# Kernel tuning notes

Measured on AMD Instinct MI355X. Metric: run time of the kernel, lower is better.

## Reference

```python
import jax, jax.numpy as jnp
import numpy as np

B, C, H, W = 16, 512, 64, 64
HEADS = 8
DIL = 2  # dilation of the 3x3 depthwise conv (padding == dilation -> shape preserving)


def setup_inputs() -> dict:
    key = jax.random.key(0)
    ks = jax.random.split(key, 4)
    x = jax.random.normal(ks[0], (B, C, H, W), jnp.float32)
    # kaiming-normal-ish scales (fan_out, relu)
    w_qkv = jax.random.normal(ks[1], (3 * C, C), jnp.float32) * (2.0 / C) ** 0.5  # 1x1 conv weight
    w_dw = jax.random.normal(ks[2], (C, 3, 3), jnp.float32) * (2.0 / 9.0) ** 0.5  # depthwise 3x3
    w_out = jax.random.normal(ks[3], (C, C), jnp.float32) * (2.0 / C) ** 0.5      # 1x1 conv weight
    temperature = jnp.sqrt(jnp.asarray(C // HEADS, jnp.float32))                  # init sqrt(dim_per_head)
    return {"x": x, "w_qkv": w_qkv, "w_dw": w_dw, "w_out": w_out, "temperature": temperature}


def _dw_conv(y, w_dw):
    # depthwise dilated 3x3 conv, padding=dilation -> same spatial size
    rhs = w_dw[:, None, :, :]  # [C,1,3,3]
    return jax.lax.conv_general_dilated(
        y, rhs, window_strides=(1, 1), padding=((DIL, DIL), (DIL, DIL)),
        rhs_dilation=(DIL, DIL), feature_group_count=y.shape[1],
        dimension_numbers=("NCHW", "OIHW", "NCHW"))


def reference(x, w_qkv, w_dw, w_out, temperature):
    b, c, h, w = x.shape
    n = h * w
    d = c // HEADS
    # 1x1 qkv projection (bias-free conv == einsum)
    qkv = jnp.einsum("oc,bchw->bohw", w_qkv, x)  # [B,3C,H,W]
    q, k, v = jnp.split(qkv, 3, axis=1)
    # same depthwise conv applied to q,k,v: fold into batch, conv once
    qkv3 = _dw_conv(jnp.concatenate([q, k, v], axis=0), w_dw)  # [3B,C,H,W]
    q, k, v = jnp.split(qkv3, 3, axis=0)
    q = q.reshape(b, HEADS, d, n)
    k = k.reshape(b, HEADS, d, n)
    v = v.reshape(b, HEADS, d, n)
    # L2 normalize along the per-head channel dim (dim=2), eps=1e-12 like F.normalize
    l2 = lambda t: t / jnp.maximum(jnp.linalg.norm(t, axis=2, keepdims=True), 1e-12)
    q = l2(q)
    k = l2(k)
    # cross-covariance attention: [B,heads,d,d]
    attn = jnp.einsum("bhdn,bhen->bhde", q, k) / jnp.maximum(temperature, 1e-5)
    attn = jax.nn.softmax(attn, axis=-1)
    # dropout is identity in eval mode
    out = jnp.einsum("bhde,bhen->bhdn", attn, v).reshape(b, c, h, w)
    return jnp.einsum("oc,bchw->bohw", w_out, out)
```

## Files before the change

kernel.cpp:

```cpp
#include <hip/hip_runtime.h>

typedef __attribute__((ext_vector_type(8))) short bf16x8;
typedef __attribute__((ext_vector_type(8))) unsigned short ushort8;
typedef __attribute__((ext_vector_type(4))) float f32x4;
typedef __attribute__((ext_vector_type(2))) float f32x2;
typedef __attribute__((ext_vector_type(4))) unsigned int u32x4;
typedef __attribute__((ext_vector_type(2))) unsigned int u32x2;

__device__ __forceinline__ float bf2f(unsigned short u) {
  union { unsigned int i; float f; } v; v.i = ((unsigned int)u) << 16; return v.f;
}
__device__ __forceinline__ float asf(unsigned int u) {
  union { unsigned int i; float f; } v; v.i = u; return v.f;
}
__device__ __forceinline__ unsigned short f2bf(float f) {
  union { float f; unsigned int i; } v; v.f = f;
  unsigned int u = v.i;
  return (unsigned short)((u + 0x7FFFu + ((u >> 16) & 1u)) >> 16);
}
__device__ __forceinline__ void gload16(const void* g, void* l) {
  __builtin_amdgcn_global_load_lds(
      (const __attribute__((address_space(1))) void*)g,
      (__attribute__((address_space(3))) void*)l, 16, 0, 0);
}

__global__ __launch_bounds__(256) void cvt_f32_bf16(const float* __restrict__ s,
                                                    unsigned short* __restrict__ d, int n) {
  int i = blockIdx.x * 256 + threadIdx.x;
  if (i < n) d[i] = f2bf(s[i]);
}

__global__ __launch_bounds__(256) void transpose_x(const float* __restrict__ x,
                                                   unsigned short* __restrict__ xt) {
  __shared__ float tile[64][65];
  const int b = blockIdx.z, ct = blockIdx.y, nt = blockIdx.x;
  const int t = threadIdx.x;
  const int r0 = t >> 6, col = t & 63;
  const float* src = x + ((size_t)b * 512 + ct * 64) * 4096 + nt * 64;
#pragma unroll
  for (int i = 0; i < 16; ++i) {
    int r = i * 4 + r0;
    tile[r][col] = src[(size_t)r * 4096 + col];
  }
  __syncthreads();
  unsigned short* dst = xt + ((size_t)b * 4096 + nt * 64) * 512 + ct * 64;
  const int c2 = (t & 31) * 2;
  const int nsub = t >> 5;
#pragma unroll
  for (int i = 0; i < 8; ++i) {
    int n = i * 8 + nsub;
    unsigned int p;
    asm("v_cvt_pk_bf16_f32 %0, %1, %2" : "=v"(p) : "v"(tile[c2][n]), "v"(tile[c2 + 1][n]));
    *(unsigned int*)(dst + (size_t)n * 512 + c2) = p;
  }
}

__global__ __launch_bounds__(512, 1) void gemm_qkv_8ph(const unsigned short* __restrict__ A,
                                                       const unsigned short* __restrict__ B,
                                                       unsigned short* __restrict__ C) {
  __shared__ unsigned short lA[2][256 * 64];
  __shared__ unsigned short lB[2][256 * 64];
  const int gx = gridDim.x;
  const int nwg = gx * gridDim.y;
  int flat = blockIdx.x + gx * blockIdx.y;
  flat = (flat & 7) * (nwg >> 3) + (flat >> 3);
  const int bx = flat % gx;
  const int by = flat / gx;
  const size_t m0 = (size_t)by * 256;
  const size_t n0 = (size_t)bx * 256;

  const int t = threadIdx.x;
  const int lane = t & 63;
  const int wid = t >> 6;
  const int wm = wid >> 2, wn = wid & 3;
  const int ro = lane & 15, kq = lane >> 4;

  const int srow = t >> 3;
  const int sslot = t & 7;
  const int kslot = sslot ^ (srow & 7);

  auto stageA = [&](int kt, int h, int bbuf) {
    char* d = (char*)(&lA[bbuf][0]) + ((h * 128 + srow) * 64 + sslot * 8) * 2;
    const unsigned short* g = A + (m0 + h * 128 + srow) * 512 + kt * 64 + kslot * 8;
    gload16(g, d);
    gload16(g + (size_t)64 * 512, d + 64 * 128);
  };
  auto stageB = [&](int kt, int h, int bbuf) {
    char* d = (char*)(&lB[bbuf][0]) + ((h * 128 + srow) * 64 + sslot * 8) * 2;
    const unsigned short* g = B + (n0 + h * 128 + srow) * 512 + kt * 64 + kslot * 8;
    gload16(g, d);
    gload16(g + (size_t)64 * 512, d + 64 * 128);
  };

  f32x4 acc[8][4] = {};

  stageA(0, 0, 0); stageA(0, 1, 0);
  stageB(0, 0, 0); stageB(0, 1, 0);
  stageA(1, 0, 1); stageA(1, 1, 1);
  asm volatile("s_waitcnt vmcnt(4)" ::: "memory");
  __builtin_amdgcn_s_barrier();

#pragma unroll 1
  for (int kt = 0; kt < 8; ++kt) {
    const int c = kt & 1;
    const unsigned short* pa = &lA[c][0];
    const unsigned short* pb = &lB[c][0];
    const int slot0 = kq ^ (ro & 7);
    const int slot1 = (4 + kq) ^ (ro & 7);

    bf16x8 a0[8], a1[8], b0, b1, b2, b3;
#pragma unroll
    for (int i = 0; i < 8; ++i)
      a0[i] = *(const bf16x8*)&pa[(wm * 128 + i * 16 + ro) * 64 + slot0 * 8];
    b0 = *(const bf16x8*)&pb[(wn * 64 + 0 * 16 + ro) * 64 + slot0 * 8];
    b1 = *(const bf16x8*)&pb[(wn * 64 + 1 * 16 + ro) * 64 + slot0 * 8];
    if (kt + 1 < 8) stageB(kt + 1, 0, c ^ 1);
    asm volatile("" ::: "memory");
    __builtin_amdgcn_s_barrier();
    asm volatile("s_waitcnt lgkmcnt(0)" ::: "memory");
    __builtin_amdgcn_s_setprio(1);
#pragma unroll
    for (int i = 0; i < 8; ++i) {
      acc[i][0] = __builtin_amdgcn_mfma_f32_16x16x32_bf16(a0[i], b0, acc[i][0], 0, 0, 0);
      acc[i][1] = __builtin_amdgcn_mfma_f32_16x16x32_bf16(a0[i], b1, acc[i][1], 0, 0, 0);
    }
    __builtin_amdgcn_s_setprio(0);

    b2 = *(const bf16x8*)&pb[(wn * 64 + 2 * 16 + ro) * 64 + slot0 * 8];
    b3 = *(const bf16x8*)&pb[(wn * 64 + 3 * 16 + ro) * 64 + slot0 * 8];
    if (kt + 1 < 8) stageB(kt + 1, 1, c ^ 1);
    asm volatile("" ::: "memory");
    __builtin_amdgcn_s_barrier();
    asm volatile("s_waitcnt lgkmcnt(0)" ::: "memory");
    __builtin_amdgcn_s_setprio(1);
#pragma unroll
    for (int i = 0; i < 8; ++i) {
      acc[i][2] = __builtin_amdgcn_mfma_f32_16x16x32_bf16(a0[i], b2, acc[i][2], 0, 0, 0);
      acc[i][3] = __builtin_amdgcn_mfma_f32_16x16x32_bf16(a0[i], b3, acc[i][3], 0, 0, 0);
    }
    __builtin_amdgcn_s_setprio(0);

#pragma unroll
    for (int i = 0; i < 8; ++i)
      a1[i] = *(const bf16x8*)&pa[(wm * 128 + i * 16 + ro) * 64 + slot1 * 8];
    b0 = *(const bf16x8*)&pb[(wn * 64 + 0 * 16 + ro) * 64 + slot1 * 8];
    b1 = *(const bf16x8*)&pb[(wn * 64 + 1 * 16 + ro) * 64 + slot1 * 8];
    asm volatile("s_waitcnt lgkmcnt(0)" ::: "memory");
    __builtin_amdgcn_s_barrier();
    __builtin_amdgcn_s_setprio(1);
#pragma unroll
    for (int i = 0; i < 8; ++i) {
      acc[i][0] = __builtin_amdgcn_mfma_f32_16x16x32_bf16(a1[i], b0, acc[i][0], 0, 0, 0);
      acc[i][1] = __builtin_amdgcn_mfma_f32_16x16x32_bf16(a1[i], b1, acc[i][1], 0, 0, 0);
    }
    __builtin_amdgcn_s_setprio(0);

    b2 = *(const bf16x8*)&pb[(wn * 64 + 2 * 16 + ro) * 64 + slot1 * 8];
    b3 = *(const bf16x8*)&pb[(wn * 64 + 3 * 16 + ro) * 64 + slot1 * 8];
    if (kt + 2 < 8) { stageA(kt + 2, 0, c); stageA(kt + 2, 1, c); }
    asm volatile("s_waitcnt lgkmcnt(0)" ::: "memory");
    if (kt < 6)       asm volatile("s_waitcnt vmcnt(4)" ::: "memory");
    else if (kt == 6) asm volatile("s_waitcnt vmcnt(0)" ::: "memory");
    __builtin_amdgcn_s_barrier();
    __builtin_amdgcn_s_setprio(1);
#pragma unroll
    for (int i = 0; i < 8; ++i) {
      acc[i][2] = __builtin_amdgcn_mfma_f32_16x16x32_bf16(a1[i], b2, acc[i][2], 0, 0, 0);
      acc[i][3] = __builtin_amdgcn_mfma_f32_16x16x32_bf16(a1[i], b3, acc[i][3], 0, 0, 0);
    }
    __builtin_amdgcn_s_setprio(0);
  }

#pragma unroll
  for (int i = 0; i < 8; ++i)
#pragma unroll
    for (int j = 0; j < 4; ++j)
#pragma unroll
      for (int r = 0; r < 4; ++r) {
        size_t row = m0 + wm * 128 + i * 16 + (kq << 2) + r;
        size_t col = n0 + wn * 64 + j * 16 + ro;
        C[row * 1536 + col] = f2bf(acc[i][j][r]);
      }
}

template <bool BF16OUT>
__global__ __launch_bounds__(256) void gemm_bt(const unsigned short* __restrict__ A,
                                               const unsigned short* __restrict__ B,
                                               void* __restrict__ Cv, int K, int ldc,
                                               size_t sA, size_t sB, size_t sC) {
  __shared__ unsigned short lA[2][128 * 32];
  __shared__ unsigned short lB[2][128 * 32];
  const int gx = gridDim.x, gy = gridDim.y;
  const int nwg = gx * gy * gridDim.z;
  int flat = blockIdx.x + gx * (blockIdx.y + gy * blockIdx.z);
  flat = (flat & 7) * (nwg >> 3) + (flat >> 3);
  const int bx = flat % gx;
  const int rem = flat / gx;
  const int by = rem % gy;
  const int bz = rem / gy;

  const int t = threadIdx.x;
  const int lane = t & 63;
  const int wv = t >> 6, wr = wv >> 1, wc = wv & 1;
  const size_t m0 = (size_t)by * 128;
  const size_t n0 = (size_t)bx * 128;
  A += (size_t)bz * sA;
  B += (size_t)bz * sB;
  const unsigned short* ga = A + (m0 + (t >> 2)) * (size_t)K + (t & 3) * 8;
  const unsigned short* gb = B + (n0 + (t >> 2)) * (size_t)K + (t & 3) * 8;
  const size_t gstep = (size_t)64 * K;

  f32x4 acc[4][4] = {};

  auto stage = [&](int kt, int bbuf) {
    const unsigned short* pa = ga + kt * 32;
    const unsigned short* pb = gb + kt * 32;
    char* da = (char*)(&lA[bbuf][0]) + t * 16;
    char* db = (char*)(&lB[bbuf][0]) + t * 16;
    gload16(pa, da);
    gload16(pa + gstep, da + 4096);
    gload16(pb, db);
    gload16(pb + gstep, db + 4096);
  };

  const int nk = K >> 5;
  stage(0, 0);
  __syncthreads();
  int buf = 0;
  for (int kt = 0; kt < nk; ++kt) {
    if (kt + 1 < nk) stage(kt + 1, buf ^ 1);
    const unsigned short* pa = &lA[buf][0];
    const unsigned short* pb = &lB[buf][0];
    const int ro = lane & 15, ko = (lane >> 4) * 8;
    bf16x8 af[4], bv[4];
#pragma unroll
    for (int i = 0; i < 4; ++i) af[i] = *(const bf16x8*)&pa[(wr * 64 + i * 16 + ro) * 32 + ko];
#pragma unroll
    for (int i = 0; i < 4; ++i) bv[i] = *(const bf16x8*)&pb[(wc * 64 + i * 16 + ro) * 32 + ko];
#pragma unroll
    for (int i = 0; i < 4; ++i)
#pragma unroll
      for (int j = 0; j < 4; ++j)
        acc[i][j] = __builtin_amdgcn_mfma_f32_16x16x32_bf16(af[i], bv[j], acc[i][j], 0, 0, 0);
    __syncthreads();
    buf ^= 1;
  }

  if constexpr (BF16OUT) {
    unsigned short* C = (unsigned short*)Cv + (size_t)bz * sC;
#pragma unroll
    for (int i = 0; i < 4; ++i)
#pragma unroll
      for (int j = 0; j < 4; ++j)
#pragma unroll
        for (int r = 0; r < 4; ++r) {
          size_t row = m0 + wr * 64 + i * 16 + ((lane >> 4) << 2) + r;
          size_t col = n0 + wc * 64 + j * 16 + (lane & 15);
          C[row * (size_t)ldc + col] = f2bf(acc[i][j][r]);
        }
  } else {
    float* C = (float*)Cv + (size_t)bz * sC;
#pragma unroll
    for (int i = 0; i < 4; ++i)
#pragma unroll
      for (int j = 0; j < 4; ++j)
#pragma unroll
        for (int r = 0; r < 4; ++r) {
          size_t row = m0 + wr * 64 + i * 16 + ((lane >> 4) << 2) + r;
          size_t col = n0 + wc * 64 + j * 16 + (lane & 15);
          C[row * (size_t)ldc + col] = acc[i][j][r];
        }
  }
}

struct Row3h { u32x2 v[3]; };

__global__ __launch_bounds__(256) void dwconv_norm(const unsigned short* __restrict__ Y,
                                                   const float* __restrict__ wdw,
                                                   unsigned short* __restrict__ Qb,
                                                   unsigned short* __restrict__ Kb,
                                                   unsigned short* __restrict__ Vb) {
  const int t = threadIdx.x, lane = t & 63, wv = t >> 6;
  const int bid = blockIdx.x;
  const int lbid = (bid & 7) * 384 + (bid >> 3);
  const int wid = lbid * 4 + wv;
  const int sub = wid & 3;
  const int x = (wid >> 2) & 63;
  const int grp = wid >> 8;
  const int par = sub >> 1, chhalf = sub & 1;
  const int b = grp / 3, part = grp - b * 3;
  const int c0 = chhalf * 256 + (lane >> 4) * 64 + (lane & 15) * 4;

  f32x2 wa[9], wb[9];
  {
    float qw[36];
    const float* wp = wdw + c0 * 9;
#pragma unroll
    for (int i = 0; i < 9; ++i) {
      f32x4 q = *(const f32x4*)(wp + i * 4);
      qw[i * 4 + 0] = q[0]; qw[i * 4 + 1] = q[1];
      qw[i * 4 + 2] = q[2]; qw[i * 4 + 3] = q[3];
    }
#pragma unroll
    for (int tap = 0; tap < 9; ++tap) {
      wa[tap] = (f32x2){qw[tap], qw[9 + tap]};
      wb[tap] = (f32x2){qw[18 + tap], qw[27 + tap]};
    }
  }

  const size_t ybase = (size_t)b * 4096 * 1536 + part * 512 + c0;
  const bool okm = (x >= 2), okp = (x <= 61);
  const int xm = okm ? x - 2 : x;
  const int xp = okp ? x + 2 : x;

  auto loadrow = [&](int yy) -> Row3h {
    Row3h r;
    const bool oky = ((unsigned)yy < 64u);
    const int yyc = oky ? yy : 0;
    const size_t rb = ybase + (size_t)(yyc * 64) * 1536;
    u32x2 a = *(const u32x2*)(Y + rb + (size_t)xm * 1536);
    u32x2 c = *(const u32x2*)(Y + rb + (size_t)x * 1536);
    u32x2 d = *(const u32x2*)(Y + rb + (size_t)xp * 1536);
    r.v[0] = a & ((oky && okm) ? 0xFFFFFFFFu : 0u);
    r.v[1] = c & (oky ? 0xFFFFFFFFu : 0u);
    r.v[2] = d & ((oky && okp) ? 0xFFFFFFFFu : 0u);
    return r;
  };

  Row3h W[4];
#pragma unroll
  for (int xt = 0; xt < 3; ++xt) W[0].v[xt] = (u32x2)(0u);
  W[1] = loadrow(par);
  W[2] = loadrow(par + 2);
  W[3] = loadrow(par + 4);

  unsigned short* dst0 = (part == 0 ? Qb : (part == 1 ? Kb : Vb)) +
                         ((size_t)b * 4096 + x) * 512 + c0;

#pragma unroll
  for (int i = 0; i < 32; ++i) {
    const int y = par + 2 * i;
    f32x2 a01 = (f32x2){0.f, 0.f}, a23 = (f32x2){0.f, 0.f};
#pragma unroll
    for (int r = 0; r < 3; ++r) {
      const Row3h& R = W[(i + r) & 3];
#pragma unroll
      for (int xt = 0; xt < 3; ++xt) {
        const int tap = r * 3 + xt;
        const u32x2 v = R.v[xt];
        f32x2 lo = (f32x2){asf(v[0] << 16), asf(v[0] & 0xFFFF0000u)};
        f32x2 hi = (f32x2){asf(v[1] << 16), asf(v[1] & 0xFFFF0000u)};
        a01 += lo * wa[tap];
        a23 += hi * wb[tap];
      }
    }
    if (part < 2) {
      f32x2 s2 = a01 * a01 + a23 * a23;
      float ss = s2[0] + s2[1];
      ss += __shfl_xor(ss, 1);
      ss += __shfl_xor(ss, 2);
      ss += __shfl_xor(ss, 4);
      ss += __shfl_xor(ss, 8);
      const float rcp = 1.f / fmaxf(sqrtf(ss), 1e-12f);
      a01 *= rcp; a23 *= rcp;
    }
    unsigned int p0, p1;
    asm("v_cvt_pk_bf16_f32 %0, %1, %2" : "=v"(p0) : "v"(a01[0]), "v"(a01[1]));
    asm("v_cvt_pk_bf16_f32 %0, %1, %2" : "=v"(p1) : "v"(a23[0]), "v"(a23[1]));
    u32x2 pk; pk[0] = p0; pk[1] = p1;
    *(u32x2*)(dst0 + (size_t)y * 64 * 512) = pk;
    if (i < 30) W[i & 3] = loadrow(y + 6);
  }
}

__global__ __launch_bounds__(256) void attn_partial(const unsigned short* __restrict__ Qb,
                                                    const unsigned short* __restrict__ Kb,
                                                    float* __restrict__ Spart) {
  __shared__ unsigned short sQ[4][64][72];
  __shared__ unsigned short sK[4][64][72];
  const int t = threadIdx.x, lane = t & 63, wv = t >> 6;
  const int bh = blockIdx.x >> 2;
  const int s = (blockIdx.x & 3) * 4 + wv;
  const int b = bh >> 3, h = bh & 7;
  const unsigned short* qbase = Qb + ((size_t)b * 4096) * 512 + h * 64;
  const unsigned short* kbase = Kb + ((size_t)b * 4096) * 512 + h * 64;
  f32x4 acc[4][4] = {};
  for (int ch = 0; ch < 4; ++ch) {
    const int n0 = s * 256 + ch * 64;
    const unsigned short* qp = qbase + (size_t)(n0 + lane) * 512;
    const unsigned short* kp = kbase + (size_t)(n0 + lane) * 512;
    ushort8 qv[8], kv[8];
#pragma unroll
    for (int v = 0; v < 8; ++v) qv[v] = *(const ushort8*)(qp + v * 8);
#pragma unroll
    for (int v = 0; v < 8; ++v) kv[v] = *(const ushort8*)(kp + v * 8);
#pragma unroll
    for (int v = 0; v < 8; ++v)
#pragma unroll
      for (int j = 0; j < 8; ++j) {
        sQ[wv][v * 8 + j][lane] = qv[v][j];
        sK[wv][v * 8 + j][lane] = kv[v][j];
      }
    __syncthreads();
    const int ro = lane & 15, ko = (lane >> 4) * 8;
#pragma unroll
    for (int ks = 0; ks < 2; ++ks) {
      bf16x8 af[4], bv[4];
#pragma unroll
      for (int i = 0; i < 4; ++i) af[i] = *(const bf16x8*)&sQ[wv][i * 16 + ro][ks * 32 + ko];
#pragma unroll
      for (int i = 0; i < 4; ++i) bv[i] = *(const bf16x8*)&sK[wv][i * 16 + ro][ks * 32 + ko];
#pragma unroll
      for (int i = 0; i < 4; ++i)
#pragma unroll
        for (int j = 0; j < 4; ++j)
          acc[i][j] = __builtin_amdgcn_mfma_f32_16x16x32_bf16(af[i], bv[j], acc[i][j], 0, 0, 0);
    }
    __syncthreads();
  }
  float* dst = Spart + ((size_t)bh * 16 + s) * 4096;
#pragma unroll
  for (int i = 0; i < 4; ++i)
#pragma unroll
    for (int j = 0; j < 4; ++j)
#pragma unroll
      for (int r = 0; r < 4; ++r) {
        int d = i * 16 + ((lane >> 4) << 2) + r;
        int e = j * 16 + (lane & 15);
        dst[d * 64 + e] = acc[i][j][r];
      }
}

__global__ __launch_bounds__(256) void softmax_attn(const float* __restrict__ Spart,
                                                    const float* __restrict__ tptr,
                                                    unsigned short* __restrict__ attn) {
  const int bh = blockIdx.x, t = threadIdx.x;
  const int d = t >> 2, eb = (t & 3) << 4;
  const float inv_t = 1.f / fmaxf(tptr[0], 1e-5f);
  float v[16];
#pragma unroll
  for (int i = 0; i < 16; ++i) v[i] = 0.f;
  for (int s = 0; s < 16; ++s) {
    const f32x4* p = (const f32x4*)(Spart + ((size_t)bh * 16 + s) * 4096 + d * 64 + eb);
#pragma unroll
    for (int i = 0; i < 4; ++i) {
      f32x4 q = p[i];
      v[i * 4 + 0] += q[0]; v[i * 4 + 1] += q[1];
      v[i * 4 + 2] += q[2]; v[i * 4 + 3] += q[3];
    }
  }
  float mx = -1e30f;
#pragma unroll
  for (int i = 0; i < 16; ++i) { v[i] *= inv_t; mx = fmaxf(mx, v[i]); }
  mx = fmaxf(mx, __shfl_xor(mx, 1));
  mx = fmaxf(mx, __shfl_xor(mx, 2));
  float sm = 0.f;
#pragma unroll
  for (int i = 0; i < 16; ++i) { v[i] = __expf(v[i] - mx); sm += v[i]; }
  sm += __shfl_xor(sm, 1);
  sm += __shfl_xor(sm, 2);
  const float r = 1.f / sm;
  ushort8 pk0, pk1;
#pragma unroll
  for (int i = 0; i < 8; ++i) { pk0[i] = f2bf(v[i] * r); pk1[i] = f2bf(v[8 + i] * r); }
  ushort8* dst = (ushort8*)(attn + (size_t)bh * 4096 + d * 64 + eb);
  dst[0] = pk0; dst[1] = pk1;
}

__global__ __launch_bounds__(256) void make_w2(const unsigned short* __restrict__ attn,
                                               const float* __restrict__ w_out,
                                               unsigned short* __restrict__ w2) {
  __shared__ float sA[4096];
  const int bx = blockIdx.x;
  const int bh = bx >> 1, half = bx & 1;
  const int b = bh >> 3, h = bh & 7;
  const int t = threadIdx.x;
  for (int i = t; i < 4096; i += 256) sA[i] = bf2f(attn[(size_t)bh * 4096 + i]);
  __syncthreads();
  const int o = half * 256 + t;
  float w[64];
  const float* wp = w_out + (size_t)o * 512 + h * 64;
#pragma unroll
  for (int i = 0; i < 64; i += 4) {
    f32x4 q = *(const f32x4*)(wp + i);
    w[i] = q[0]; w[i + 1] = q[1]; w[i + 2] = q[2]; w[i + 3] = q[3];
  }
  unsigned short* dst = w2 + ((size_t)b * 512 + o) * 512 + h * 64;
#pragma unroll 1
  for (int eg = 0; eg < 8; ++eg) {
    ushort8 pk;
#pragma unroll
    for (int ee = 0; ee < 8; ++ee) {
      const int e = eg * 8 + ee;
      float acc = 0.f;
#pragma unroll
      for (int dd = 0; dd < 64; ++dd) acc += w[dd] * sA[dd * 64 + e];
      pk[ee] = f2bf(acc);
    }
    *(ushort8*)(dst + eg * 8) = pk;
  }
}

extern "C" void kernel_launch(void* const* d_in, const int* in_sizes, int n_in,
                              void* d_out, int out_size, void* d_ws, size_t ws_size,
                              hipStream_t stream) {
  const float* x     = (const float*)d_in[0];
  const float* w_qkv = (const float*)d_in[1];
  const float* w_dw  = (const float*)d_in[2];
  const float* w_out = (const float*)d_in[3];
  const float* temp  = (const float*)d_in[4];
  float* out = (float*)d_out;

  char* ws = (char*)d_ws;
  const size_t MB = 1024 * 1024;
  unsigned short* Xt    = (unsigned short*)(ws);
  float*          Spart = (float*)(ws);
  unsigned short* attn  = (unsigned short*)(ws + 32 * MB);
  unsigned short* w2    = (unsigned short*)(ws + 33 * MB);
  unsigned short* Y     = (unsigned short*)(ws + 64 * MB);
  unsigned short* Qb    = (unsigned short*)(ws + 256 * MB);
  unsigned short* Kb    = (unsigned short*)(ws + 320 * MB);
  unsigned short* Vb    = (unsigned short*)(ws + 384 * MB);
  unsigned short* Wq    = (unsigned short*)(ws + 448 * MB);

  cvt_f32_bf16<<<3072, 256, 0, stream>>>(w_qkv, Wq, 1536 * 512);
  transpose_x<<<dim3(64, 8, 16), 256, 0, stream>>>(x, Xt);
  gemm_qkv_8ph<<<dim3(6, 256), 512, 0, stream>>>(Xt, Wq, Y);
  dwconv_norm<<<3072, 256, 0, stream>>>(Y, w_dw, Qb, Kb, Vb);
  attn_partial<<<512, 256, 0, stream>>>(Qb, Kb, Spart);
  softmax_attn<<<128, 256, 0, stream>>>(Spart, temp, attn);
  make_w2<<<256, 256, 0, stream>>>(attn, w_out, w2);
  gemm_bt<false><<<dim3(32, 4, 16), 256, 0, stream>>>(
      w2, Vb, out, 512, 4096,
      (size_t)512 * 512, (size_t)4096 * 512, (size_t)512 * 4096);
}
```

Baseline: 413.0 us.

## Compute two dilated-conv columns per wave to share horizontal tap loads

Each wave in the depthwise dilated conv now produces two output columns (x0 and x0+2) over half the rows, loading four input columns per row instead of three per column. Horizontal input reuse cuts global loads per output from 3 to 2 per row, and the split into row halves keeps the total wave count the same. In exchange each lane holds more live registers (two accumulator sets, 12 loaded vectors) and needs extra halo row loads at each row-half boundary.

```diff
diff --git a/kernel.cpp b/kernel.cpp
--- a/kernel.cpp
+++ b/kernel.cpp
@@ -273,7 +273,7 @@
   }
 }
 
-struct Row3h { u32x2 v[3]; };
+struct Row4 { u32x2 v[4]; };
 
 __global__ __launch_bounds__(256) void dwconv_norm(const unsigned short* __restrict__ Y,
                                                    const float* __restrict__ wdw,
@@ -284,11 +284,12 @@
   const int bid = blockIdx.x;
   const int lbid = (bid & 7) * 384 + (bid >> 3);
   const int wid = lbid * 4 + wv;
-  const int sub = wid & 3;
-  const int x = (wid >> 2) & 63;
+  const int sub = wid & 255;
   const int grp = wid >> 8;
-  const int par = sub >> 1, chhalf = sub & 1;
+  const int pair = sub >> 3;
+  const int par = (sub >> 2) & 1, chhalf = (sub >> 1) & 1, rowhalf = sub & 1;
   const int b = grp / 3, part = grp - b * 3;
+  const int x0 = (pair >> 1) * 4 + (pair & 1);
   const int c0 = chhalf * 256 + (lane >> 4) * 64 + (lane & 15) * 4;
 
   f32x2 wa[9], wb[9];
@@ -309,67 +310,86 @@
   }
 
   const size_t ybase = (size_t)b * 4096 * 1536 + part * 512 + c0;
-  const bool okm = (x >= 2), okp = (x <= 61);
-  const int xm = okm ? x - 2 : x;
-  const int xp = okp ? x + 2 : x;
-
-  auto loadrow = [&](int yy) -> Row3h {
-    Row3h r;
+  const bool okm = (x0 >= 2), okp = (x0 + 4 <= 63);
+  const int cm = okm ? x0 - 2 : x0;
+  const int cp = okp ? x0 + 4 : x0;
+
+  auto loadrow = [&](int yy) -> Row4 {
+    Row4 r;
     const bool oky = ((unsigned)yy < 64u);
     const int yyc = oky ? yy : 0;
     const size_t rb = ybase + (size_t)(yyc * 64) * 1536;
-    u32x2 a = *(const u32x2*)(Y + rb + (size_t)xm * 1536);
-    u32x2 c = *(const u32x2*)(Y + rb + (size_t)x * 1536);
-    u32x2 d = *(const u32x2*)(Y + rb + (size_t)xp * 1536);
+    u32x2 a = *(const u32x2*)(Y + rb + (size_t)cm * 1536);
+    u32x2 c = *(const u32x2*)(Y + rb + (size_t)x0 * 1536);
+    u32x2 d = *(const u32x2*)(Y + rb + (size_t)(x0 + 2) * 1536);
+    u32x2 e = *(const u32x2*)(Y + rb + (size_t)cp * 1536);
     r.v[0] = a & ((oky && okm) ? 0xFFFFFFFFu : 0u);
     r.v[1] = c & (oky ? 0xFFFFFFFFu : 0u);
-    r.v[2] = d & ((oky && okp) ? 0xFFFFFFFFu : 0u);
+    r.v[2] = d & (oky ? 0xFFFFFFFFu : 0u);
+    r.v[3] = e & ((oky && okp) ? 0xFFFFFFFFu : 0u);
     return r;
   };
 
-  Row3h W[4];
-#pragma unroll
-  for (int xt = 0; xt < 3; ++xt) W[0].v[xt] = (u32x2)(0u);
-  W[1] = loadrow(par);
-  W[2] = loadrow(par + 2);
-  W[3] = loadrow(par + 4);
-
-  unsigned short* dst0 = (part == 0 ? Qb : (part == 1 ? Kb : Vb)) +
-                         ((size_t)b * 4096 + x) * 512 + c0;
-
-#pragma unroll
-  for (int i = 0; i < 32; ++i) {
-    const int y = par + 2 * i;
-    f32x2 a01 = (f32x2){0.f, 0.f}, a23 = (f32x2){0.f, 0.f};
+  const int y0 = par + rowhalf * 32;
+  Row4 W[3];
+  W[0] = loadrow(y0 - 2);
+  W[1] = loadrow(y0);
+  W[2] = loadrow(y0 + 2);
+
+  unsigned short* dstA = (part == 0 ? Qb : (part == 1 ? Kb : Vb)) +
+                         ((size_t)b * 4096 + x0) * 512 + c0;
+  unsigned short* dstB = dstA + (size_t)2 * 512;
+
+#pragma unroll
+  for (int i = 0; i < 16; ++i) {
+    const int y = y0 + 2 * i;
+    f32x2 A01 = (f32x2){0.f, 0.f}, A23 = (f32x2){0.f, 0.f};
+    f32x2 B01 = (f32x2){0.f, 0.f}, B23 = (f32x2){0.f, 0.f};
 #pragma unroll
     for (int r = 0; r < 3; ++r) {
-      const Row3h& R = W[(i + r) & 3];
-#pragma unroll
-      for (int xt = 0; xt < 3; ++xt) {
-        const int tap = r * 3 + xt;
+      const Row4& R = W[(i + r) % 3];
+#pragma unroll
+      for (int xt = 0; xt < 4; ++xt) {
         const u32x2 v = R.v[xt];
         f32x2 lo = (f32x2){asf(v[0] << 16), asf(v[0] & 0xFFFF0000u)};
         f32x2 hi = (f32x2){asf(v[1] << 16), asf(v[1] & 0xFFFF0000u)};
-        a01 += lo * wa[tap];
-        a23 += hi * wb[tap];
+        if (xt < 3) {
+          const int tap = r * 3 + xt;
+          A01 += lo * wa[tap];
+          A23 += hi * wb[tap];
+        }
+        if (xt >= 1) {
+          const int tap = r * 3 + xt - 1;
+          B01 += lo * wa[tap];
+          B23 += hi * wb[tap];
+        }
       }
     }
     if (part < 2) {
-      f32x2 s2 = a01 * a01 + a23 * a23;
-      float ss = s2[0] + s2[1];
-      ss += __shfl_xor(ss, 1);
-      ss += __shfl_xor(ss, 2);
-      ss += __shfl_xor(ss, 4);
-      ss += __shfl_xor(ss, 8);
-      const float rcp = 1.f / fmaxf(sqrtf(ss), 1e-12f);
-      a01 *= rcp; a23 *= rcp;
-    }
-    unsigned int p0, p1;
-    asm("v_cvt_pk_bf16_f32 %0, %1, %2" : "=v"(p0) : "v"(a01[0]), "v"(a01[1]));
-    asm("v_cvt_pk_bf16_f32 %0, %1, %2" : "=v"(p1) : "v"(a23[0]), "v"(a23[1]));
-    u32x2 pk; pk[0] = p0; pk[1] = p1;
-    *(u32x2*)(dst0 + (size_t)y * 64 * 512) = pk;
-    if (i < 30) W[i & 3] = loadrow(y + 6);
+      f32x2 sa = A01 * A01 + A23 * A23;
+      f32x2 sb = B01 * B01 + B23 * B23;
+      float ssa = sa[0] + sa[1];
+      float ssb = sb[0] + sb[1];
+#pragma unroll
+      for (int m = 1; m <= 8; m <<= 1) {
+        ssa += __shfl_xor(ssa, m);
+        ssb += __shfl_xor(ssb, m);
+      }
+      const float ra = 1.f / fmaxf(sqrtf(ssa), 1e-12f);
+      const float rb2 = 1.f / fmaxf(sqrtf(ssb), 1e-12f);
+      A01 *= ra; A23 *= ra;
+      B01 *= rb2; B23 *= rb2;
+    }
+    unsigned int p0, p1, q0, q1;
+    asm("v_cvt_pk_bf16_f32 %0, %1, %2" : "=v"(p0) : "v"(A01[0]), "v"(A01[1]));
+    asm("v_cvt_pk_bf16_f32 %0, %1, %2" : "=v"(p1) : "v"(A23[0]), "v"(A23[1]));
+    asm("v_cvt_pk_bf16_f32 %0, %1, %2" : "=v"(q0) : "v"(B01[0]), "v"(B01[1]));
+    asm("v_cvt_pk_bf16_f32 %0, %1, %2" : "=v"(q1) : "v"(B23[0]), "v"(B23[1]));
+    u32x2 pkA; pkA[0] = p0; pkA[1] = p1;
+    u32x2 pkB; pkB[0] = q0; pkB[1] = q1;
+    *(u32x2*)(dstA + (size_t)y * 64 * 512) = pkA;
+    *(u32x2*)(dstB + (size_t)y * 64 * 512) = pkB;
+    if (i < 15) W[i % 3] = loadrow(y + 4);
   }
 }
 
```

After: 403.3 us. -2.3%, faster.

## Reuse 256x256 8-phase GEMM for output projection and widen dwconv per-thread tiles

Applied to the files above, without the earlier changes.

The final batched output GEMM now runs on the 256x256 eight-phase pipelined MFMA kernel used for the QKV projection, replacing the simpler 128x128 double-buffered kernel, which was generalised with batch strides and an fp32 output path. The depthwise conv kernel now has each wave compute four output columns (stride two) over half the rows, loading six input columns per row so neighbouring taps are shared and redundant global loads drop. The grid is halved to match. The trade-offs are more registers per thread in the conv and fewer workgroups for the output GEMM (512), which may lower occupancy and load balance.

```diff
diff --git a/kernel.cpp b/kernel.cpp
--- a/kernel.cpp
+++ b/kernel.cpp
@@ -55,19 +55,25 @@
   }
 }
 
-__global__ __launch_bounds__(512, 1) void gemm_qkv_8ph(const unsigned short* __restrict__ A,
-                                                       const unsigned short* __restrict__ B,
-                                                       unsigned short* __restrict__ C) {
+template <bool BF16OUT>
+__global__ __launch_bounds__(512, 1) void gemm256_8ph(const unsigned short* __restrict__ A,
+                                                      const unsigned short* __restrict__ B,
+                                                      void* __restrict__ Cv, int ldc,
+                                                      size_t sA, size_t sB, size_t sC) {
   __shared__ unsigned short lA[2][256 * 64];
   __shared__ unsigned short lB[2][256 * 64];
-  const int gx = gridDim.x;
-  const int nwg = gx * gridDim.y;
-  int flat = blockIdx.x + gx * blockIdx.y;
+  const int gx = gridDim.x, gy = gridDim.y;
+  const int nwg = gx * gy * gridDim.z;
+  int flat = blockIdx.x + gx * (blockIdx.y + gy * blockIdx.z);
   flat = (flat & 7) * (nwg >> 3) + (flat >> 3);
   const int bx = flat % gx;
-  const int by = flat / gx;
+  const int rem = flat / gx;
+  const int by = rem % gy;
+  const int bz = rem / gy;
   const size_t m0 = (size_t)by * 256;
   const size_t n0 = (size_t)bx * 256;
+  A += (size_t)bz * sA;
+  B += (size_t)bz * sB;
 
   const int t = threadIdx.x;
   const int lane = t & 63;
@@ -171,109 +177,34 @@
     __builtin_amdgcn_s_setprio(0);
   }
 
-#pragma unroll
-  for (int i = 0; i < 8; ++i)
-#pragma unroll
-    for (int j = 0; j < 4; ++j)
-#pragma unroll
-      for (int r = 0; r < 4; ++r) {
-        size_t row = m0 + wm * 128 + i * 16 + (kq << 2) + r;
-        size_t col = n0 + wn * 64 + j * 16 + ro;
-        C[row * 1536 + col] = f2bf(acc[i][j][r]);
-      }
-}
-
-template <bool BF16OUT>
-__global__ __launch_bounds__(256) void gemm_bt(const unsigned short* __restrict__ A,
-                                               const unsigned short* __restrict__ B,
-                                               void* __restrict__ Cv, int K, int ldc,
-                                               size_t sA, size_t sB, size_t sC) {
-  __shared__ unsigned short lA[2][128 * 32];
-  __shared__ unsigned short lB[2][128 * 32];
-  const int gx = gridDim.x, gy = gridDim.y;
-  const int nwg = gx * gy * gridDim.z;
-  int flat = blockIdx.x + gx * (blockIdx.y + gy * blockIdx.z);
-  flat = (flat & 7) * (nwg >> 3) + (flat >> 3);
-  const int bx = flat % gx;
-  const int rem = flat / gx;
-  const int by = rem % gy;
-  const int bz = rem / gy;
-
-  const int t = threadIdx.x;
-  const int lane = t & 63;
-  const int wv = t >> 6, wr = wv >> 1, wc = wv & 1;
-  const size_t m0 = (size_t)by * 128;
-  const size_t n0 = (size_t)bx * 128;
-  A += (size_t)bz * sA;
-  B += (size_t)bz * sB;
-  const unsigned short* ga = A + (m0 + (t >> 2)) * (size_t)K + (t & 3) * 8;
-  const unsigned short* gb = B + (n0 + (t >> 2)) * (size_t)K + (t & 3) * 8;
-  const size_t gstep = (size_t)64 * K;
-
-  f32x4 acc[4][4] = {};
-
-  auto stage = [&](int kt, int bbuf) {
-    const unsigned short* pa = ga + kt * 32;
-    const unsigned short* pb = gb + kt * 32;
-    char* da = (char*)(&lA[bbuf][0]) + t * 16;
-    char* db = (char*)(&lB[bbuf][0]) + t * 16;
-    gload16(pa, da);
-    gload16(pa + gstep, da + 4096);
-    gload16(pb, db);
-    gload16(pb + gstep, db + 4096);
-  };
-
-  const int nk = K >> 5;
-  stage(0, 0);
-  __syncthreads();
-  int buf = 0;
-  for (int kt = 0; kt < nk; ++kt) {
-    if (kt + 1 < nk) stage(kt + 1, buf ^ 1);
-    const unsigned short* pa = &lA[buf][0];
-    const unsigned short* pb = &lB[buf][0];
-    const int ro = lane & 15, ko = (lane >> 4) * 8;
-    bf16x8 af[4], bv[4];
-#pragma unroll
-    for (int i = 0; i < 4; ++i) af[i] = *(const bf16x8*)&pa[(wr * 64 + i * 16 + ro) * 32 + ko];
-#pragma unroll
-    for (int i = 0; i < 4; ++i) bv[i] = *(const bf16x8*)&pb[(wc * 64 + i * 16 + ro) * 32 + ko];
-#pragma unroll
-    for (int i = 0; i < 4; ++i)
+  if constexpr (BF16OUT) {
+    unsigned short* C = (unsigned short*)Cv + (size_t)0 * sC;
+#pragma unroll
+    for (int i = 0; i < 8; ++i)
 #pragma unroll
       for (int j = 0; j < 4; ++j)
-        acc[i][j] = __builtin_amdgcn_mfma_f32_16x16x32_bf16(af[i], bv[j], acc[i][j], 0, 0, 0);
-    __syncthreads();
-    buf ^= 1;
-  }
-
-  if constexpr (BF16OUT) {
-    unsigned short* C = (unsigned short*)Cv + (size_t)bz * sC;
-#pragma unroll
-    for (int i = 0; i < 4; ++i)
-#pragma unroll
-      for (int j = 0; j < 4; ++j)
 #pragma unroll
         for (int r = 0; r < 4; ++r) {
-          size_t row = m0 + wr * 64 + i * 16 + ((lane >> 4) << 2) + r;
-          size_t col = n0 + wc * 64 + j * 16 + (lane & 15);
+          size_t row = m0 + wm * 128 + i * 16 + (kq << 2) + r;
+          size_t col = n0 + wn * 64 + j * 16 + ro;
           C[row * (size_t)ldc + col] = f2bf(acc[i][j][r]);
         }
   } else {
     float* C = (float*)Cv + (size_t)bz * sC;
 #pragma unroll
-    for (int i = 0; i < 4; ++i)
+    for (int i = 0; i < 8; ++i)
 #pragma unroll
       for (int j = 0; j < 4; ++j)
 #pragma unroll
         for (int r = 0; r < 4; ++r) {
-          size_t row = m0 + wr * 64 + i * 16 + ((lane >> 4) << 2) + r;
-          size_t col = n0 + wc * 64 + j * 16 + (lane & 15);
+          size_t row = m0 + wm * 128 + i * 16 + (kq << 2) + r;
+          size_t col = n0 + wn * 64 + j * 16 + ro;
           C[row * (size_t)ldc + col] = acc[i][j][r];
         }
   }
 }
 
-struct Row3h { u32x2 v[3]; };
+struct Row6 { u32x2 v[6]; };
 
 __global__ __launch_bounds__(256) void dwconv_norm(const unsigned short* __restrict__ Y,
                                                    const float* __restrict__ wdw,
@@ -282,13 +213,14 @@
                                                    unsigned short* __restrict__ Vb) {
   const int t = threadIdx.x, lane = t & 63, wv = t >> 6;
   const int bid = blockIdx.x;
-  const int lbid = (bid & 7) * 384 + (bid >> 3);
+  const int lbid = (bid & 7) * 192 + (bid >> 3);
   const int wid = lbid * 4 + wv;
-  const int sub = wid & 3;
-  const int x = (wid >> 2) & 63;
-  const int grp = wid >> 8;
-  const int par = sub >> 1, chhalf = sub & 1;
+  const int sub = wid & 127;
+  const int grp = wid >> 7;
+  const int base = sub >> 3;
+  const int par = (sub >> 2) & 1, chhalf = (sub >> 1) & 1, rowhalf = sub & 1;
   const int b = grp / 3, part = grp - b * 3;
+  const int x0 = (base >> 1) * 8 + (base & 1);
   const int c0 = chhalf * 256 + (lane >> 4) * 64 + (lane & 15) * 4;
 
   f32x2 wa[9], wb[9];
@@ -309,67 +241,80 @@
   }
 
   const size_t ybase = (size_t)b * 4096 * 1536 + part * 512 + c0;
-  const bool okm = (x >= 2), okp = (x <= 61);
-  const int xm = okm ? x - 2 : x;
-  const int xp = okp ? x + 2 : x;
-
-  auto loadrow = [&](int yy) -> Row3h {
-    Row3h r;
+  const bool okm = (x0 >= 2), okp = (x0 + 8 <= 63);
+  int xc[6];
+  xc[0] = okm ? x0 - 2 : x0;
+#pragma unroll
+  for (int j = 1; j < 5; ++j) xc[j] = x0 - 2 + 2 * j;
+  xc[5] = okp ? x0 + 8 : x0;
+
+  auto loadrow = [&](int yy) -> Row6 {
+    Row6 r;
     const bool oky = ((unsigned)yy < 64u);
     const int yyc = oky ? yy : 0;
     const size_t rb = ybase + (size_t)(yyc * 64) * 1536;
-    u32x2 a = *(const u32x2*)(Y + rb + (size_t)xm * 1536);
-    u32x2 c = *(const u32x2*)(Y + rb + (size_t)x * 1536);
-    u32x2 d = *(const u32x2*)(Y + rb + (size_t)xp * 1536);
-    r.v[0] = a & ((oky && okm) ? 0xFFFFFFFFu : 0u);
-    r.v[1] = c & (oky ? 0xFFFFFFFFu : 0u);
-    r.v[2] = d & ((oky && okp) ? 0xFFFFFFFFu : 0u);
+#pragma unroll
+    for (int j = 0; j < 6; ++j) {
+      u32x2 v = *(const u32x2*)(Y + rb + (size_t)xc[j] * 1536);
+      bool ok = oky && !(j == 0 && !okm) && !(j == 5 && !okp);
+      r.v[j] = v & (ok ? 0xFFFFFFFFu : 0u);
+    }
     return r;
   };
 
-  Row3h W[4];
-#pragma unroll
-  for (int xt = 0; xt < 3; ++xt) W[0].v[xt] = (u32x2)(0u);
-  W[1] = loadrow(par);
-  W[2] = loadrow(par + 2);
-  W[3] = loadrow(par + 4);
+  const int y0 = par + rowhalf * 32;
+  Row6 W[3];
+  W[0] = loadrow(y0 - 2);
+  W[1] = loadrow(y0);
+  W[2] = loadrow(y0 + 2);
 
   unsigned short* dst0 = (part == 0 ? Qb : (part == 1 ? Kb : Vb)) +
-                         ((size_t)b * 4096 + x) * 512 + c0;
-
-#pragma unroll
-  for (int i = 0; i < 32; ++i) {
-    const int y = par + 2 * i;
-    f32x2 a01 = (f32x2){0.f, 0.f}, a23 = (f32x2){0.f, 0.f};
+                         ((size_t)b * 4096 + x0) * 512 + c0;
+
+#pragma unroll
+  for (int i = 0; i < 16; ++i) {
+    const int y = y0 + 2 * i;
+    f32x2 A01[4], A23[4];
+#pragma unroll
+    for (int o = 0; o < 4; ++o) { A01[o] = (f32x2){0.f, 0.f}; A23[o] = (f32x2){0.f, 0.f}; }
 #pragma unroll
     for (int r = 0; r < 3; ++r) {
-      const Row3h& R = W[(i + r) & 3];
-#pragma unroll
-      for (int xt = 0; xt < 3; ++xt) {
-        const int tap = r * 3 + xt;
-        const u32x2 v = R.v[xt];
+      const Row6& R = W[(i + r) % 3];
+#pragma unroll
+      for (int j = 0; j < 6; ++j) {
+        const u32x2 v = R.v[j];
         f32x2 lo = (f32x2){asf(v[0] << 16), asf(v[0] & 0xFFFF0000u)};
         f32x2 hi = (f32x2){asf(v[1] << 16), asf(v[1] & 0xFFFF0000u)};
-        a01 += lo * wa[tap];
-        a23 += hi * wb[tap];
+#pragma unroll
+        for (int o = 0; o < 4; ++o) {
+          const int xt = j - o;
+          if (xt >= 0 && xt < 3) {
+            const int tap = r * 3 + xt;
+            A01[o] += lo * wa[tap];
+            A23[o] += hi * wb[tap];
+          }
+        }
       }
     }
-    if (part < 2) {
-      f32x2 s2 = a01 * a01 + a23 * a23;
-      float ss = s2[0] + s2[1];
-      ss += __shfl_xor(ss, 1);
-      ss += __shfl_xor(ss, 2);
-      ss += __shfl_xor(ss, 4);
-      ss += __shfl_xor(ss, 8);
-      const float rcp = 1.f / fmaxf(sqrtf(ss), 1e-12f);
-      a01 *= rcp; a23 *= rcp;
-    }
-    unsigned int p0, p1;
-    asm("v_cvt_pk_bf16_f32 %0, %1, %2" : "=v"(p0) : "v"(a01[0]), "v"(a01[1]));
-    asm("v_cvt_pk_bf16_f32 %0, %1, %2" : "=v"(p1) : "v"(a23[0]), "v"(a23[1]));
-    u32x2 pk; pk[0] = p0; pk[1] = p1;
-    *(u32x2*)(dst0 + (size_t)y * 64 * 512) = pk;
-    if (i < 30) W[i & 3] = loadrow(y + 6);
+#pragma unroll
+    for (int o = 0; o < 4; ++o) {
+      if (part < 2) {
+        f32x2 s2 = A01[o] * A01[o] + A23[o] * A23[o];
+        float ss = s2[0] + s2[1];
+        ss += __shfl_xor(ss, 1);
+        ss += __shfl_xor(ss, 2);
+        ss += __shfl_xor(ss, 4);
+        ss += __shfl_xor(ss, 8);
+        const float rcp = 1.f / fmaxf(sqrtf(ss), 1e-12f);
+        A01[o] *= rcp; A23[o] *= rcp;
+      }
+      unsigned int p0, p1;
+      asm("v_cvt_pk_bf16_f32 %0, %1, %2" : "=v"(p0) : "v"(A01[o][0]), "v"(A01[o][1]));
+      asm("v_cvt_pk_bf16_f32 %0, %1, %2" : "=v"(p1) : "v"(A23[o][0]), "v"(A23[o][1]));
+      u32x2 pk; pk[0] = p0; pk[1] = p1;
+      *(u32x2*)(dst0 + ((size_t)y * 64 + 2 * o) * 512) = pk;
+    }
+    if (i < 15) W[i % 3] = loadrow(y + 4);
   }
 }
 
@@ -525,12 +470,12 @@
 
   cvt_f32_bf16<<<3072, 256, 0, stream>>>(w_qkv, Wq, 1536 * 512);
   transpose_x<<<dim3(64, 8, 16), 256, 0, stream>>>(x, Xt);
-  gemm_qkv_8ph<<<dim3(6, 256), 512, 0, stream>>>(Xt, Wq, Y);
-  dwconv_norm<<<3072, 256, 0, stream>>>(Y, w_dw, Qb, Kb, Vb);
+  gemm256_8ph<true><<<dim3(6, 256, 1), 512, 0, stream>>>(Xt, Wq, Y, 1536, 0, 0, 0);
+  dwconv_norm<<<1536, 256, 0, stream>>>(Y, w_dw, Qb, Kb, Vb);
   attn_partial<<<512, 256, 0, stream>>>(Qb, Kb, Spart);
   softmax_attn<<<128, 256, 0, stream>>>(Spart, temp, attn);
   make_w2<<<256, 256, 0, stream>>>(attn, w_out, w2);
-  gemm_bt<false><<<dim3(32, 4, 16), 256, 0, stream>>>(
-      w2, Vb, out, 512, 4096,
+  gemm256_8ph<false><<<dim3(16, 2, 16), 512, 0, stream>>>(
+      w2, Vb, out, 4096,
       (size_t)512 * 512, (size_t)4096 * 512, (size_t)512 * 4096);
 }
```

After: 412.1 us. About the same (-0.2%).
